# Kernel tuning notes

Hardware: AMD Instinct MI355X
Metric: run time of the kernel (lower is better)

Reference implementation:

```python
import jax, jax.numpy as jnp
import numpy as np

B, S, DIN, D = 16, 1024, 64, 64

def setup_inputs() -> dict:
    key = jax.random.key(0)
    kx, kq, kk, kv, kaK, kaV = jax.random.split(key, 6)
    w_scale = 1.0 / np.sqrt(DIN)
    x = jax.random.normal(kx, (B, S, DIN), dtype=jnp.float32)
    Wq = jax.random.normal(kq, (DIN, D), dtype=jnp.float32) * w_scale
    Wk = jax.random.normal(kk, (DIN, D), dtype=jnp.float32) * w_scale
    Wv = jax.random.normal(kv, (DIN, D), dtype=jnp.float32) * w_scale
    # relative-position bias tables alpha_K/alpha_V: [S, S, D]
    alpha_K = jax.random.normal(kaK, (S, S, D), dtype=jnp.float32) * 0.02
    alpha_V = jax.random.normal(kaV, (S, S, D), dtype=jnp.float32) * 0.02
    return {"x": x, "Wq": Wq, "Wk": Wk, "Wv": Wv,
            "alpha_K": alpha_K, "alpha_V": alpha_V}

def reference(x, Wq, Wk, Wv, alpha_K, alpha_V):
    # Relation-aware self-attention (Shaw et al. style), vectorized form of
    # the original per-query loop:
    #   score[b,i,j] = q[b,i] . (k[b,j] + alpha_K[i,j]) / sqrt(D)
    #   z[b,i]       = sum_j softmax_j(score)[b,i,j] * (v[b,j] + alpha_V[i,j])
    d = Wq.shape[1]
    inv_sqrt_d = 1.0 / np.sqrt(d)
    q = jnp.einsum('bsf,fd->bsd', x, Wq)
    k = jnp.einsum('bsf,fd->bsd', x, Wk)
    v = jnp.einsum('bsf,fd->bsd', x, Wv)
    scores = (jnp.einsum('bid,bjd->bij', q, k)
              + jnp.einsum('bid,ijd->bij', q, alpha_K)) * inv_sqrt_d
    attn = jax.nn.softmax(scores, axis=-1)  # [B, S, S]
    z = (jnp.einsum('bij,bjd->bid', attn, v)
         + jnp.einsum('bij,ijd->bid', attn, alpha_V))
    return z, attn
```

## Files before the change

### kernel.cpp

```cpp
#include <hip/hip_runtime.h>
#include <hip/hip_fp16.h>
#include <hip/hip_bf16.h>


typedef unsigned short u16;
typedef __attribute__((ext_vector_type(8))) short bhalf8;
typedef __attribute__((ext_vector_type(4))) short bhalf4;
typedef __attribute__((ext_vector_type(4))) float fx4;

#if defined(__has_builtin)
#if __has_builtin(__builtin_amdgcn_mfma_f32_16x16x16bf16_1k)
#define HAS_MFMA16 1
#endif
#endif

__device__ __forceinline__ void bar_lds() {
  asm volatile("s_waitcnt lgkmcnt(0)" ::: "memory");
  __builtin_amdgcn_s_barrier();
}

__device__ __forceinline__ short b16(float f) {
  __hip_bfloat16 h = __float2bfloat16(f);
  return *reinterpret_cast<short*>(&h);
}
__device__ __forceinline__ float bf2f(short s) {
  union { unsigned u; float f; } v; v.u = ((unsigned)(u16)s) << 16; return v.f;
}
__device__ __forceinline__ bhalf4 pk4(float4 a) {
  bhalf4 r; r[0] = b16(a.x); r[1] = b16(a.y); r[2] = b16(a.z); r[3] = b16(a.w); return r;
}
__device__ __forceinline__ bhalf8 pack8(float4 a, float4 b) {
  bhalf8 r;
  r[0] = b16(a.x); r[1] = b16(a.y); r[2] = b16(a.z); r[3] = b16(a.w);
  r[4] = b16(b.x); r[5] = b16(b.y); r[6] = b16(b.z); r[7] = b16(b.w);
  return r;
}

__global__ __launch_bounds__(256) void k_proj(
    const float* __restrict__ x, const float* __restrict__ Wq,
    const float* __restrict__ Wk, const float* __restrict__ Wv,
    u16* __restrict__ qbf, u16* __restrict__ kbf, float* __restrict__ vf)
{
  __shared__ float wl[3 * 4096];
  const int t = threadIdx.x;
  for (int c = t; c < 4096; c += 256) {
    wl[c] = Wq[c]; wl[4096 + c] = Wk[c]; wl[8192 + c] = Wv[c];
  }
  __syncthreads();
  const int row = blockIdx.x * 64 + (t >> 2);
  const int dbase = (t & 3) * 16;
  float xr[64];
  const float4* xp = (const float4*)(x + (size_t)row * 64);
#pragma unroll
  for (int c = 0; c < 16; ++c) {
    float4 v = xp[c];
    xr[4*c] = v.x; xr[4*c+1] = v.y; xr[4*c+2] = v.z; xr[4*c+3] = v.w;
  }
  float aq[16], ak[16], av[16];
#pragma unroll
  for (int m = 0; m < 16; ++m) { aq[m] = 0.f; ak[m] = 0.f; av[m] = 0.f; }
#pragma unroll
  for (int f = 0; f < 64; ++f) {
    const float xv = xr[f];
    const float* wq = wl + f * 64 + dbase;
#pragma unroll
    for (int m = 0; m < 16; ++m) {
      aq[m] = fmaf(xv, wq[m], aq[m]);
      ak[m] = fmaf(xv, wq[4096 + m], ak[m]);
      av[m] = fmaf(xv, wq[8192 + m], av[m]);
    }
  }
  union { u16 u[16]; uint4 q[2]; } pq, pk;
#pragma unroll
  for (int m = 0; m < 16; ++m) { pq.u[m] = (u16)b16(aq[m]); pk.u[m] = (u16)b16(ak[m]); }
  const size_t o = (size_t)row * 64 + dbase;
  *(uint4*)(qbf + o) = pq.q[0]; *(uint4*)(qbf + o + 8) = pq.q[1];
  *(uint4*)(kbf + o) = pk.q[0]; *(uint4*)(kbf + o + 8) = pk.q[1];
  float4* vo = (float4*)(vf + o);
  vo[0] = make_float4(av[0], av[1], av[2], av[3]);
  vo[1] = make_float4(av[4], av[5], av[6], av[7]);
  vo[2] = make_float4(av[8], av[9], av[10], av[11]);
  vo[3] = make_float4(av[12], av[13], av[14], av[15]);
}

__global__ __launch_bounds__(256) void k_qk(
    const u16* __restrict__ qbf, const u16* __restrict__ kbf, __half* __restrict__ qkw)
{
  const int t = threadIdx.x, l = t & 63, w = t >> 6;
  const int bq = blockIdx.x & 15, it = blockIdx.x >> 4;
  const int lr = l & 15, lg = l >> 4;
  const int i0 = it * 64 + w * 16;
  const u16* qp = qbf + (size_t)(bq * 1024 + i0 + lr) * 64 + lg * 8;
  bhalf8 a0 = *(const bhalf8*)(qp);
  bhalf8 a1 = *(const bhalf8*)(qp + 32);
  auto ldK = [&](int jt, bhalf8& b0, bhalf8& b1) {
    const u16* kp = kbf + (size_t)(bq * 1024 + jt * 16 + lr) * 64 + lg * 8;
    b0 = *(const bhalf8*)(kp);
    b1 = *(const bhalf8*)(kp + 32);
  };
  auto doK = [&](int jt, bhalf8 b0, bhalf8 b1) {
    fx4 acc = {0.f, 0.f, 0.f, 0.f};
    acc = __builtin_amdgcn_mfma_f32_16x16x32_bf16(a0, b0, acc, 0, 0, 0);
    acc = __builtin_amdgcn_mfma_f32_16x16x32_bf16(a1, b1, acc, 0, 0, 0);
#pragma unroll
    for (int r = 0; r < 4; ++r) {
      const int i = i0 + lg * 4 + r;
      qkw[((size_t)i * 16 + bq) * 1024 + jt * 16 + lr] = __float2half(acc[r]);
    }
  };
  bhalf8 k0a, k0b, k1a, k1b, k2a, k2b, k3a, k3b;
  ldK(0, k0a, k0b); ldK(1, k1a, k1b); ldK(2, k2a, k2b); ldK(3, k3a, k3b);
#pragma unroll
  for (int jt = 0; jt < 64; jt += 4) {
    doK(jt + 0, k0a, k0b); if (jt + 4 < 64) ldK(jt + 4, k0a, k0b);
    doK(jt + 1, k1a, k1b); if (jt + 5 < 64) ldK(jt + 5, k1a, k1b);
    doK(jt + 2, k2a, k2b); if (jt + 6 < 64) ldK(jt + 6, k2a, k2b);
    doK(jt + 3, k3a, k3b); if (jt + 7 < 64) ldK(jt + 7, k3a, k3b);
  }
}

#define SLD2 516
#define PADJ 40
__global__ __launch_bounds__(256, 4) void k_core(
    const float* __restrict__ aK, const float* __restrict__ aV,
    const u16* __restrict__ qbf, const __half* __restrict__ qkw,
    float* __restrict__ attn_out, float* __restrict__ za)
{
  __shared__ __align__(16) float sl[16 * SLD2];
  __shared__ __align__(16) u16 vt[64 * PADJ];
  __shared__ float stats[64];
  const int i = blockIdx.x;
  const int t = threadIdx.x, l = t & 63, w = t >> 6;
  const int lr = l & 15, lg = l >> 4;
  const int jj = l >> 2;
  const int cc = (l & 3) * 4;

#ifdef HAS_MFMA16
  const u16* qrow = qbf + (size_t)(lr * 1024 + i) * 64;
  bhalf4 aq0 = *(const bhalf4*)(qrow + 0  + lg * 4);
  bhalf4 aq1 = *(const bhalf4*)(qrow + 16 + lg * 4);
  bhalf4 aq2 = *(const bhalf4*)(qrow + 32 + lg * 4);
  bhalf4 aq3 = *(const bhalf4*)(qrow + 48 + lg * 4);
#else
  const u16* qp = qbf + (size_t)(lr * 1024 + i) * 64 + lg * 8;
  bhalf8 a0 = *(const bhalf8*)(qp);
  bhalf8 a1 = *(const bhalf8*)(qp + 32);
#endif

  fx4 zacc = {0.f, 0.f, 0.f, 0.f};
  bhalf4 e1b0[4], e1b1[4];

#pragma unroll
  for (int h = 0; h < 2; ++h) {
    const float* avbase = aV + ((size_t)i * 1024 + h * 512) * 64 + w * 16 + cc;
    auto ldC = [&](int it, float4& pa, float4& pb) {
      const float* nb = avbase + (size_t)(it * 32) * 64;
      pa = *(const float4*)(nb + (size_t)jj * 64);
      pb = *(const float4*)(nb + (size_t)(jj + 16) * 64);
    };
    float4 p0a, p0b, p1a, p1b, p2a, p2b, p3a, p3b;
    ldC(0, p0a, p0b); ldC(1, p1a, p1b); ldC(2, p2a, p2b); ldC(3, p3a, p3b);

#ifdef HAS_MFMA16
    const float* baseA = aK + ((size_t)i * 1024 + h * 512 + lr) * 64 + lg * 4;
    auto ldA = [&](int tt, float4* c) {
      const float* p = baseA + (size_t)((w + tt * 4) * 16) * 64;
      c[0] = *(const float4*)(p);
      c[1] = *(const float4*)(p + 16);
      c[2] = *(const float4*)(p + 32);
      c[3] = *(const float4*)(p + 48);
    };
    auto doA = [&](int tt, const float4* c) {
      fx4 acc = {0.f, 0.f, 0.f, 0.f};
      acc = __builtin_amdgcn_mfma_f32_16x16x16bf16_1k(aq0, pk4(c[0]), acc, 0, 0, 0);
      acc = __builtin_amdgcn_mfma_f32_16x16x16bf16_1k(aq1, pk4(c[1]), acc, 0, 0, 0);
      acc = __builtin_amdgcn_mfma_f32_16x16x16bf16_1k(aq2, pk4(c[2]), acc, 0, 0, 0);
      acc = __builtin_amdgcn_mfma_f32_16x16x16bf16_1k(aq3, pk4(c[3]), acc, 0, 0, 0);
      const int j0 = (w + tt * 4) * 16;
#pragma unroll
      for (int r = 0; r < 4; ++r)
        sl[(lg * 4 + r) * SLD2 + j0 + lr] = acc[r];
    };
#else
    const float* baseA = aK + ((size_t)i * 1024 + h * 512 + lr) * 64 + lg * 8;
    auto ldA = [&](int tt, float4* c) {
      const float* p = baseA + (size_t)((w + tt * 4) * 16) * 64;
      c[0] = *(const float4*)(p);
      c[1] = *(const float4*)(p + 4);
      c[2] = *(const float4*)(p + 32);
      c[3] = *(const float4*)(p + 36);
    };
    auto doA = [&](int tt, const float4* c) {
      fx4 acc = {0.f, 0.f, 0.f, 0.f};
      acc = __builtin_amdgcn_mfma_f32_16x16x32_bf16(a0, pack8(c[0], c[1]), acc, 0, 0, 0);
      acc = __builtin_amdgcn_mfma_f32_16x16x32_bf16(a1, pack8(c[2], c[3]), acc, 0, 0, 0);
      const int j0 = (w + tt * 4) * 16;
#pragma unroll
      for (int r = 0; r < 4; ++r)
        sl[(lg * 4 + r) * SLD2 + j0 + lr] = acc[r];
    };
#endif
    float4 cA[4], cB[4];
    ldA(0, cA); ldA(1, cB);
#pragma unroll
    for (int tt = 0; tt < 8; tt += 2) {
      doA(tt, cA);     if (tt + 2 < 8) ldA(tt + 2, cA);
      doA(tt + 1, cB); if (tt + 3 < 8) ldA(tt + 3, cB);
    }

    uint2 qv0[4], qv1[4];
#pragma unroll
    for (int rr = 0; rr < 4; ++rr) {
      const __half* qb = qkw + ((size_t)i * 16 + w * 4 + rr) * 1024 + h * 512;
      qv0[rr] = *(const uint2*)(qb + l * 4);
      qv1[rr] = *(const uint2*)(qb + 256 + l * 4);
    }
    bar_lds();

    if (h == 0) {
#pragma unroll
      for (int rr = 0; rr < 4; ++rr) {
        const int row = w * 4 + rr;
        float* rp = sl + row * SLD2;
        float2 g0 = __half22float2(((const __half2*)&qv0[rr])[0]);
        float2 g1 = __half22float2(((const __half2*)&qv0[rr])[1]);
        float2 g2 = __half22float2(((const __half2*)&qv1[rr])[0]);
        float2 g3 = __half22float2(((const __half2*)&qv1[rr])[1]);
        float4 x0 = *(const float4*)(rp + l * 4);
        float4 x1 = *(const float4*)(rp + 256 + l * 4);
        float v8[8] = {x0.x + g0.x, x0.y + g0.y, x0.z + g1.x, x0.w + g1.y,
                       x1.x + g2.x, x1.y + g2.y, x1.z + g3.x, x1.w + g3.y};
        float mx = -3.0e30f;
#pragma unroll
        for (int c = 0; c < 8; ++c) mx = fmaxf(mx, v8[c]);
#pragma unroll
        for (int off = 32; off; off >>= 1) mx = fmaxf(mx, __shfl_xor(mx, off));
        float e8[8]; float sum = 0.f;
#pragma unroll
        for (int c = 0; c < 8; ++c) { e8[c] = __expf((v8[c] - mx) * 0.125f); sum += e8[c]; }
        bhalf4 eh0 = pk4(make_float4(e8[0], e8[1], e8[2], e8[3]));
        bhalf4 eh1 = pk4(make_float4(e8[4], e8[5], e8[6], e8[7]));
        *(bhalf4*)((u16*)rp + l * 4)       = eh0;
        *(bhalf4*)((u16*)rp + 256 + l * 4) = eh1;
        e1b0[rr] = eh0; e1b1[rr] = eh1;
#pragma unroll
        for (int off = 32; off; off >>= 1) sum += __shfl_xor(sum, off);
        if (l == 0) { stats[row] = mx; stats[16 + row] = sum; }
      }
    } else {
#pragma unroll
      for (int rr = 0; rr < 4; ++rr) {
        const int row = w * 4 + rr;
        float* rp = sl + row * SLD2;
        float2 g0 = __half22float2(((const __half2*)&qv0[rr])[0]);
        float2 g1 = __half22float2(((const __half2*)&qv0[rr])[1]);
        float2 g2 = __half22float2(((const __half2*)&qv1[rr])[0]);
        float2 g3 = __half22float2(((const __half2*)&qv1[rr])[1]);
        float4 x0 = *(const float4*)(rp + l * 4);
        float4 x1 = *(const float4*)(rp + 256 + l * 4);
        float v8[8] = {x0.x + g0.x, x0.y + g0.y, x0.z + g1.x, x0.w + g1.y,
                       x1.x + g2.x, x1.y + g2.y, x1.z + g3.x, x1.w + g3.y};
        float mx = -3.0e30f;
#pragma unroll
        for (int c = 0; c < 8; ++c) mx = fmaxf(mx, v8[c]);
#pragma unroll
        for (int off = 32; off; off >>= 1) mx = fmaxf(mx, __shfl_xor(mx, off));
        const float m1 = stats[row];
        const float m  = fmaxf(m1, mx);
        const float corr = __expf((m1 - m) * 0.125f);
        float e8[8]; float sum = 0.f;
#pragma unroll
        for (int c = 0; c < 8; ++c) { e8[c] = __expf((v8[c] - m) * 0.125f); sum += e8[c]; }
        bhalf4 eh0 = pk4(make_float4(e8[0], e8[1], e8[2], e8[3]));
        bhalf4 eh1 = pk4(make_float4(e8[4], e8[5], e8[6], e8[7]));
        *(bhalf4*)((u16*)rp + l * 4)       = eh0;
        *(bhalf4*)((u16*)rp + 256 + l * 4) = eh1;
#pragma unroll
        for (int off = 32; off; off >>= 1) sum += __shfl_xor(sum, off);
        const float inv = 1.0f / (stats[16 + row] * corr + sum);
        float* ao1 = attn_out + ((size_t)row * 1024 + i) * 1024 + 512;
        *(float4*)(ao1 + l * 4)       = make_float4(e8[0]*inv, e8[1]*inv, e8[2]*inv, e8[3]*inv);
        *(float4*)(ao1 + 256 + l * 4) = make_float4(e8[4]*inv, e8[5]*inv, e8[6]*inv, e8[7]*inv);
        const float f = corr * inv;
        float* ao0 = attn_out + ((size_t)row * 1024 + i) * 1024;
        *(float4*)(ao0 + l * 4)       = make_float4(bf2f(e1b0[rr][0])*f, bf2f(e1b0[rr][1])*f,
                                                    bf2f(e1b0[rr][2])*f, bf2f(e1b0[rr][3])*f);
        *(float4*)(ao0 + 256 + l * 4) = make_float4(bf2f(e1b1[rr][0])*f, bf2f(e1b1[rr][1])*f,
                                                    bf2f(e1b1[rr][2])*f, bf2f(e1b1[rr][3])*f);
        if (l == 0) { stats[32 + row] = corr; stats[48 + row] = inv; }
      }
    }
    bar_lds();

    if (h == 1) {
#pragma unroll
      for (int r = 0; r < 4; ++r) zacc[r] *= stats[32 + lg * 4 + r];
    }
    u16* vtw = vt + (size_t)(w * 16 + cc) * PADJ + jj;
    const u16* vtr = vt + (size_t)(w * 16 + lr) * PADJ + lg * 8;
    const u16* slr = (const u16*)(sl + (size_t)lr * SLD2);
    auto doC = [&](int it, float4 ca, float4 cb) {
      vtw[0 * PADJ]      = (u16)b16(ca.x);
      vtw[1 * PADJ]      = (u16)b16(ca.y);
      vtw[2 * PADJ]      = (u16)b16(ca.z);
      vtw[3 * PADJ]      = (u16)b16(ca.w);
      vtw[0 * PADJ + 16] = (u16)b16(cb.x);
      vtw[1 * PADJ + 16] = (u16)b16(cb.y);
      vtw[2 * PADJ + 16] = (u16)b16(cb.z);
      vtw[3 * PADJ + 16] = (u16)b16(cb.w);
      bhalf8 ea = *(const bhalf8*)(slr + it * 32 + lg * 8);
      bhalf8 bv = *(const bhalf8*)(vtr);
      zacc = __builtin_amdgcn_mfma_f32_16x16x32_bf16(ea, bv, zacc, 0, 0, 0);
    };
#pragma unroll
    for (int it = 0; it < 16; it += 4) {
      doC(it + 0, p0a, p0b); if (it + 4 < 16) ldC(it + 4, p0a, p0b);
      doC(it + 1, p1a, p1b); if (it + 5 < 16) ldC(it + 5, p1a, p1b);
      doC(it + 2, p2a, p2b); if (it + 6 < 16) ldC(it + 6, p2a, p2b);
      doC(it + 3, p3a, p3b); if (it + 7 < 16) ldC(it + 7, p3a, p3b);
    }
    bar_lds();
  }

#pragma unroll
  for (int r = 0; r < 4; ++r) {
    const int b = lg * 4 + r;
    za[((size_t)i * 16 + b) * 64 + w * 16 + lr] = zacc[r] * stats[48 + b];
  }
}

__global__ __launch_bounds__(256) void k_zv(
    const float* __restrict__ attn, const float* __restrict__ vf,
    const float* __restrict__ za, float* __restrict__ zout)
{
  __shared__ __align__(16) u16 vt[64 * PADJ];
  const int t = threadIdx.x, l = t & 63, w = t >> 6;
  const int b = blockIdx.x & 15, it16 = blockIdx.x >> 4;
  const int lr = l & 15, lg = l >> 4;
  const int i0 = it16 * 16;
  const int jj = l >> 2;
  const int cc = (l & 3) * 4;
  const float* vbase = vf + (size_t)b * 65536 + w * 16 + cc;
  float zr[4];
#pragma unroll
  for (int r = 0; r < 4; ++r)
    zr[r] = za[((size_t)(i0 + lg * 4 + r) * 16 + b) * 64 + w * 16 + lr];
  fx4 acc = {0.f, 0.f, 0.f, 0.f};
  u16* vtw = vt + (size_t)(w * 16 + cc) * PADJ + jj;
  auto ldV = [&](int jt, float4& pa, float4& pb) {
    const float* nb = vbase + (size_t)(jt * 32) * 64;
    pa = *(const float4*)(nb + (size_t)jj * 64);
    pb = *(const float4*)(nb + (size_t)(jj + 16) * 64);
  };
#ifdef HAS_MFMA16
  const float* abase = attn + ((size_t)(b * 1024 + i0 + lr)) * 1024 + lg * 4;
  auto ldAt = [&](int jt, float4& t0, float4& t1) {
    const float* p = abase + jt * 32;
    t0 = *(const float4*)(p);
    t1 = *(const float4*)(p + 16);
  };
#else
  const float* abase = attn + ((size_t)(b * 1024 + i0 + lr)) * 1024 + lg * 8;
  auto ldAt = [&](int jt, float4& t0, float4& t1) {
    const float* p = abase + jt * 32;
    t0 = *(const float4*)(p);
    t1 = *(const float4*)(p + 4);
  };
#endif
  auto doT = [&](float4 va, float4 vb, float4 t0, float4 t1) {
    vtw[0 * PADJ]      = (u16)b16(va.x);
    vtw[1 * PADJ]      = (u16)b16(va.y);
    vtw[2 * PADJ]      = (u16)b16(va.z);
    vtw[3 * PADJ]      = (u16)b16(va.w);
    vtw[0 * PADJ + 16] = (u16)b16(vb.x);
    vtw[1 * PADJ + 16] = (u16)b16(vb.y);
    vtw[2 * PADJ + 16] = (u16)b16(vb.z);
    vtw[3 * PADJ + 16] = (u16)b16(vb.w);
#ifdef HAS_MFMA16
    bhalf4 bv0 = *(const bhalf4*)(vt + (size_t)(w * 16 + lr) * PADJ + lg * 4);
    bhalf4 bv1 = *(const bhalf4*)(vt + (size_t)(w * 16 + lr) * PADJ + 16 + lg * 4);
    acc = __builtin_amdgcn_mfma_f32_16x16x16bf16_1k(pk4(t0), bv0, acc, 0, 0, 0);
    acc = __builtin_amdgcn_mfma_f32_16x16x16bf16_1k(pk4(t1), bv1, acc, 0, 0, 0);
#else
    bhalf8 af = pack8(t0, t1);
    bhalf8 bv = *(const bhalf8*)(vt + (size_t)(w * 16 + lr) * PADJ + lg * 8);
    acc = __builtin_amdgcn_mfma_f32_16x16x32_bf16(af, bv, acc, 0, 0, 0);
#endif
  };
  float4 v0a, v0b, v1a, v1b, v2a, v2b, v3a, v3b;
  float4 a0_, a1_, b0_, b1_, c0_, c1_, d0_, d1_;
  ldV(0, v0a, v0b); ldAt(0, a0_, a1_);
  ldV(1, v1a, v1b); ldAt(1, b0_, b1_);
  ldV(2, v2a, v2b); ldAt(2, c0_, c1_);
  ldV(3, v3a, v3b); ldAt(3, d0_, d1_);
#pragma unroll
  for (int jt = 0; jt < 32; jt += 4) {
    doT(v0a, v0b, a0_, a1_); if (jt + 4 < 32) { ldV(jt + 4, v0a, v0b); ldAt(jt + 4, a0_, a1_); }
    doT(v1a, v1b, b0_, b1_); if (jt + 5 < 32) { ldV(jt + 5, v1a, v1b); ldAt(jt + 5, b0_, b1_); }
    doT(v2a, v2b, c0_, c1_); if (jt + 6 < 32) { ldV(jt + 6, v2a, v2b); ldAt(jt + 6, c0_, c1_); }
    doT(v3a, v3b, d0_, d1_); if (jt + 7 < 32) { ldV(jt + 7, v3a, v3b); ldAt(jt + 7, d0_, d1_); }
  }
#pragma unroll
  for (int r = 0; r < 4; ++r)
    zout[((size_t)b * 1024 + i0 + lg * 4 + r) * 64 + w * 16 + lr] = acc[r] + zr[r];
}

extern "C" void kernel_launch(void* const* d_in, const int* in_sizes, int n_in,
                              void* d_out, int out_size, void* d_ws, size_t ws_size,
                              hipStream_t stream)
{
  const float* x  = (const float*)d_in[0];
  const float* Wq = (const float*)d_in[1];
  const float* Wk = (const float*)d_in[2];
  const float* Wv = (const float*)d_in[3];
  const float* aK = (const float*)d_in[4];
  const float* aV = (const float*)d_in[5];
  float* zout = (float*)d_out;
  float* attn_out = zout + (size_t)16 * 1024 * 64;

  char* ws = (char*)d_ws;
  u16*    qbf = (u16*)(ws);
  u16*    kbf = (u16*)(ws + (size_t)2  * 1024 * 1024);
  float*  vf  = (float*)(ws + (size_t)4  * 1024 * 1024);
  float*  za  = (float*)(ws + (size_t)8  * 1024 * 1024);
  __half* qkw = (__half*)(ws + (size_t)12 * 1024 * 1024);

  hipLaunchKernelGGL(k_proj, dim3(256),  dim3(256), 0, stream, x, Wq, Wk, Wv, qbf, kbf, vf);
  hipLaunchKernelGGL(k_qk,   dim3(256),  dim3(256), 0, stream, qbf, kbf, qkw);
  hipLaunchKernelGGL(k_core, dim3(1024), dim3(256), 0, stream, aK, aV, qbf, qkw, attn_out, za);
  hipLaunchKernelGGL(k_zv,   dim3(1024), dim3(256), 0, stream, attn_out, vf, za, zout);
}
```

Baseline: 216.7 us.

## Stream alpha_K tiles into LDS via global_load_lds double buffering

Replaces the per-thread register loads of alpha_K with direct global-to-LDS DMA (global_load_lds, 16 bytes per lane) into a double-buffered 64x64 shared tile, with vmcnt waits and barriers per chunk. The q·alpha_K MFMA then reads from LDS. The alpha_V prefetch loads move to after the softmax phase instead of being issued up front. The aim is to cut VGPR pressure and overlap alpha_K streaming with compute. In exchange it adds 32KB of LDS per block, which may lower occupancy below the 4-block launch bound, plus two barriers per chunk.

Result: no change. 220.2 us (+1.6%).

```diff
diff --git a/kernel.cpp b/kernel.cpp
--- a/kernel.cpp
+++ b/kernel.cpp
@@ -17,6 +17,12 @@
 __device__ __forceinline__ void bar_lds() {
   asm volatile("s_waitcnt lgkmcnt(0)" ::: "memory");
   __builtin_amdgcn_s_barrier();
+}
+
+__device__ __forceinline__ void dma16(const float* g, void* l) {
+  __builtin_amdgcn_global_load_lds(
+      (const __attribute__((address_space(1))) void*)g,
+      (__attribute__((address_space(3))) void*)l, 16, 0, 0);
 }
 
 __device__ __forceinline__ short b16(float f) {
@@ -127,6 +133,7 @@
     float* __restrict__ attn_out, float* __restrict__ za)
 {
   __shared__ __align__(16) float sl[16 * SLD2];
+  __shared__ __align__(16) float aks[2][64 * 64];
   __shared__ __align__(16) u16 vt[64 * PADJ];
   __shared__ float stats[64];
   const int i = blockIdx.x;
@@ -135,78 +142,16 @@
   const int jj = l >> 2;
   const int cc = (l & 3) * 4;
 
-#ifdef HAS_MFMA16
-  const u16* qrow = qbf + (size_t)(lr * 1024 + i) * 64;
-  bhalf4 aq0 = *(const bhalf4*)(qrow + 0  + lg * 4);
-  bhalf4 aq1 = *(const bhalf4*)(qrow + 16 + lg * 4);
-  bhalf4 aq2 = *(const bhalf4*)(qrow + 32 + lg * 4);
-  bhalf4 aq3 = *(const bhalf4*)(qrow + 48 + lg * 4);
-#else
   const u16* qp = qbf + (size_t)(lr * 1024 + i) * 64 + lg * 8;
   bhalf8 a0 = *(const bhalf8*)(qp);
   bhalf8 a1 = *(const bhalf8*)(qp + 32);
-#endif
 
   fx4 zacc = {0.f, 0.f, 0.f, 0.f};
   bhalf4 e1b0[4], e1b1[4];
 
 #pragma unroll
   for (int h = 0; h < 2; ++h) {
-    const float* avbase = aV + ((size_t)i * 1024 + h * 512) * 64 + w * 16 + cc;
-    auto ldC = [&](int it, float4& pa, float4& pb) {
-      const float* nb = avbase + (size_t)(it * 32) * 64;
-      pa = *(const float4*)(nb + (size_t)jj * 64);
-      pb = *(const float4*)(nb + (size_t)(jj + 16) * 64);
-    };
-    float4 p0a, p0b, p1a, p1b, p2a, p2b, p3a, p3b;
-    ldC(0, p0a, p0b); ldC(1, p1a, p1b); ldC(2, p2a, p2b); ldC(3, p3a, p3b);
-
-#ifdef HAS_MFMA16
-    const float* baseA = aK + ((size_t)i * 1024 + h * 512 + lr) * 64 + lg * 4;
-    auto ldA = [&](int tt, float4* c) {
-      const float* p = baseA + (size_t)((w + tt * 4) * 16) * 64;
-      c[0] = *(const float4*)(p);
-      c[1] = *(const float4*)(p + 16);
-      c[2] = *(const float4*)(p + 32);
-      c[3] = *(const float4*)(p + 48);
-    };
-    auto doA = [&](int tt, const float4* c) {
-      fx4 acc = {0.f, 0.f, 0.f, 0.f};
-      acc = __builtin_amdgcn_mfma_f32_16x16x16bf16_1k(aq0, pk4(c[0]), acc, 0, 0, 0);
-      acc = __builtin_amdgcn_mfma_f32_16x16x16bf16_1k(aq1, pk4(c[1]), acc, 0, 0, 0);
-      acc = __builtin_amdgcn_mfma_f32_16x16x16bf16_1k(aq2, pk4(c[2]), acc, 0, 0, 0);
-      acc = __builtin_amdgcn_mfma_f32_16x16x16bf16_1k(aq3, pk4(c[3]), acc, 0, 0, 0);
-      const int j0 = (w + tt * 4) * 16;
-#pragma unroll
-      for (int r = 0; r < 4; ++r)
-        sl[(lg * 4 + r) * SLD2 + j0 + lr] = acc[r];
-    };
-#else
-    const float* baseA = aK + ((size_t)i * 1024 + h * 512 + lr) * 64 + lg * 8;
-    auto ldA = [&](int tt, float4* c) {
-      const float* p = baseA + (size_t)((w + tt * 4) * 16) * 64;
-      c[0] = *(const float4*)(p);
-      c[1] = *(const float4*)(p + 4);
-      c[2] = *(const float4*)(p + 32);
-      c[3] = *(const float4*)(p + 36);
-    };
-    auto doA = [&](int tt, const float4* c) {
-      fx4 acc = {0.f, 0.f, 0.f, 0.f};
-      acc = __builtin_amdgcn_mfma_f32_16x16x32_bf16(a0, pack8(c[0], c[1]), acc, 0, 0, 0);
-      acc = __builtin_amdgcn_mfma_f32_16x16x32_bf16(a1, pack8(c[2], c[3]), acc, 0, 0, 0);
-      const int j0 = (w + tt * 4) * 16;
-#pragma unroll
-      for (int r = 0; r < 4; ++r)
-        sl[(lg * 4 + r) * SLD2 + j0 + lr] = acc[r];
-    };
-#endif
-    float4 cA[4], cB[4];
-    ldA(0, cA); ldA(1, cB);
-#pragma unroll
-    for (int tt = 0; tt < 8; tt += 2) {
-      doA(tt, cA);     if (tt + 2 < 8) ldA(tt + 2, cA);
-      doA(tt + 1, cB); if (tt + 3 < 8) ldA(tt + 3, cB);
-    }
+    const size_t baseAK = ((size_t)i * 1024 + h * 512) * 64;
 
     uint2 qv0[4], qv1[4];
 #pragma unroll
@@ -215,7 +160,41 @@
       qv0[rr] = *(const uint2*)(qb + l * 4);
       qv1[rr] = *(const uint2*)(qb + 256 + l * 4);
     }
-    bar_lds();
+
+    auto issue_chunk = [&](int c, int bb) {
+#pragma unroll
+      for (int k4 = 0; k4 < 4; ++k4) {
+        const int k = w * 4 + k4;
+        const float* src = aK + baseAK + (size_t)(c * 64 + k * 4 + (l >> 4)) * 64 + (l & 15) * 4;
+        dma16(src, &aks[bb][k * 256]);
+      }
+    };
+    issue_chunk(0, 0);
+#pragma unroll
+    for (int c = 0; c < 8; ++c) {
+      if (c < 7) {
+        issue_chunk(c + 1, (c + 1) & 1);
+        asm volatile("s_waitcnt vmcnt(4)" ::: "memory");
+      } else {
+        asm volatile("s_waitcnt vmcnt(0)" ::: "memory");
+      }
+      __builtin_amdgcn_s_barrier();
+      __builtin_amdgcn_sched_barrier(0);
+      const float* tb = aks[c & 1] + (size_t)(w * 16 + lr) * 64 + lg * 8;
+      float4 c0 = *(const float4*)(tb);
+      float4 c1 = *(const float4*)(tb + 4);
+      float4 c2 = *(const float4*)(tb + 32);
+      float4 c3 = *(const float4*)(tb + 36);
+      fx4 acc = {0.f, 0.f, 0.f, 0.f};
+      acc = __builtin_amdgcn_mfma_f32_16x16x32_bf16(a0, pack8(c0, c1), acc, 0, 0, 0);
+      acc = __builtin_amdgcn_mfma_f32_16x16x32_bf16(a1, pack8(c2, c3), acc, 0, 0, 0);
+      const int j0 = c * 64 + w * 16;
+#pragma unroll
+      for (int r = 0; r < 4; ++r)
+        sl[(lg * 4 + r) * SLD2 + j0 + lr] = acc[r];
+      asm volatile("s_waitcnt lgkmcnt(0)" ::: "memory");
+      __builtin_amdgcn_s_barrier();
+    }
 
     if (h == 0) {
 #pragma unroll
@@ -296,6 +275,12 @@
 #pragma unroll
       for (int r = 0; r < 4; ++r) zacc[r] *= stats[32 + lg * 4 + r];
     }
+    const float* avbase = aV + ((size_t)i * 1024 + h * 512) * 64 + w * 16 + cc;
+    auto ldC = [&](int it, float4& pa, float4& pb) {
+      const float* nb = avbase + (size_t)(it * 32) * 64;
+      pa = *(const float4*)(nb + (size_t)jj * 64);
+      pb = *(const float4*)(nb + (size_t)(jj + 16) * 64);
+    };
     u16* vtw = vt + (size_t)(w * 16 + cc) * PADJ + jj;
     const u16* vtr = vt + (size_t)(w * 16 + lr) * PADJ + lg * 8;
     const u16* slr = (const u16*)(sl + (size_t)lr * SLD2);
@@ -312,6 +297,8 @@
       bhalf8 bv = *(const bhalf8*)(vtr);
       zacc = __builtin_amdgcn_mfma_f32_16x16x32_bf16(ea, bv, zacc, 0, 0, 0);
     };
+    float4 p0a, p0b, p1a, p1b, p2a, p2b, p3a, p3b;
+    ldC(0, p0a, p0b); ldC(1, p1a, p1b); ldC(2, p2a, p2b); ldC(3, p3a, p3b);
 #pragma unroll
     for (int it = 0; it < 16; it += 4) {
       doC(it + 0, p0a, p0b); if (it + 4 < 16) ldC(it + 4, p0a, p0b);
```
